# Optimization experiments

Measured on AMD Instinct MI355X. Metric: run time of the kernel, lower is better.

## Reference

```python
import jax, jax.numpy as jnp
import numpy as np

EPS = float(np.finfo(np.float32).eps)
FFT_SIZE, HOP, WIN = 1024, 120, 600
ANCHOR, KF = 7, 7
LRELU_SLOPE = 0.1

def make_log_shift(anchor=ANCHOR, kf=KF, out_scale=1000.0, in_scale=0.001):
    s = (np.arange(kf) + 1) / anchor
    ls = out_scale * np.log(in_scale * s)
    ls -= ls[anchor - 1]
    return -ls  # positive, monotonically decreasing to 0 at the anchor tap

SHIFTS = make_log_shift()

def stft_mag(y):
    # y: (B, T) -> (B, 513, n_frames), matches torch.stft(center=True, reflect)
    B, T = y.shape
    pad = FFT_SIZE // 2
    yp = jnp.pad(y, ((0, 0), (pad, pad)), mode='reflect')
    n_frames = 1 + (T + 2 * pad - FFT_SIZE) // HOP
    idx = jnp.arange(n_frames)[:, None] * HOP + jnp.arange(FFT_SIZE)[None, :]
    frames = yp[:, idx]                                  # (B, n_frames, fft)
    n = np.arange(WIN)
    w = 0.5 * (1.0 - np.cos(2.0 * np.pi * n / WIN))      # periodic Hann(600)
    lp = (FFT_SIZE - WIN) // 2                           # centered pad to fft
    w = jnp.asarray(np.pad(w, (lp, FFT_SIZE - WIN - lp)), dtype=y.dtype)
    spec = jnp.fft.rfft(frames * w, axis=-1)
    mag = jnp.sqrt(jnp.clip(spec.real ** 2 + spec.imag ** 2, EPS))
    return jnp.transpose(mag, (0, 2, 1))

def int_shift(x, k):
    # output[..., f, :] = x[..., f-k, :], zero-fill; k >= 0 (static python int)
    F = x.shape[2]
    if k == 0:
        return x
    if k >= F:
        return jnp.zeros_like(x)
    return jnp.pad(x[:, :, :F - k, :], ((0, 0), (0, 0), (k, 0), (0, 0)))

def frac_shift(x, s):
    # linear-interpolation frequency shift (= interp_shift CUDA kernel)
    if s == int(s):
        return int_shift(x, int(s))
    s0 = int(np.floor(s)); frac = float(s - s0)
    return (1.0 - frac) * int_shift(x, s0) + frac * int_shift(x, s0 + 1)

def wnorm(v, g):
    # weight_norm: w = g * v / ||v|| (norm over all dims but out-channel)
    n = jnp.sqrt(jnp.sum(v * v, axis=(1, 2, 3), keepdims=True))
    return g * v / n

def conv2d(x, w, b, stride, padding):
    out = jax.lax.conv_general_dilated(
        x, w, window_strides=stride,
        padding=((padding[0], padding[0]), (padding[1], padding[1])),
        dimension_numbers=('NCHW', 'OIHW', 'NCHW'))
    return out + b[None, :, None, None]

def lrelu(x):
    return jax.nn.leaky_relu(x, LRELU_SLOPE)

def harmonic_conv(x, v, g, b):
    # x: (B,1,F,T). Log-harmonic lowering: stack 7 fractionally-shifted copies
    lowered = jnp.concatenate([frac_shift(x, SHIFTS[fk]) for fk in range(KF)], axis=1)
    w = wnorm(v, g)                                      # (32, 7, 1, 7)
    return conv2d(lowered, w, b, (1, 1), (0, 3))         # padding[0] forced to 0

def setup_inputs() -> dict:
    key = jax.random.key(0)
    ks = jax.random.split(key, 16)
    p = {}
    p['y'] = jax.random.normal(ks[0], (4, 1, 96000), dtype=jnp.float32)
    p['v0'] = jax.random.normal(ks[1], (32, 7, 1, 7), dtype=jnp.float32) * 0.05
    p['g0'] = jnp.ones((32, 1, 1, 1), dtype=jnp.float32)
    p['b0'] = jnp.zeros((32,), dtype=jnp.float32)
    for i, kk in zip((1, 2, 3), (2, 3, 4)):
        p[f'v{i}'] = jax.random.normal(ks[kk], (32, 32, 3, 9), dtype=jnp.float32) * 0.05
        p[f'g{i}'] = jnp.ones((32, 1, 1, 1), dtype=jnp.float32)
        p[f'b{i}'] = jnp.zeros((32,), dtype=jnp.float32)
    p['v4'] = jax.random.normal(ks[5], (32, 32, 3, 3), dtype=jnp.float32) * 0.05
    p['g4'] = jnp.ones((32, 1, 1, 1), dtype=jnp.float32)
    p['b4'] = jnp.zeros((32,), dtype=jnp.float32)
    p['vo'] = jax.random.normal(ks[6], (1, 32, 3, 3), dtype=jnp.float32) * 0.05
    p['go'] = jnp.ones((1, 1, 1, 1), dtype=jnp.float32)
    p['bo'] = jnp.zeros((1,), dtype=jnp.float32)
    return p

def reference(y, v0, g0, b0, v1, g1, b1, v2, g2, b2, v3, g3, b3,
              v4, g4, b4, vo, go, bo):
    mag = stft_mag(y[:, 0, :])          # (B, 513, frames)
    x = mag[:, None]                    # (B, 1, 513, frames)
    fmap = []
    x = lrelu(harmonic_conv(x, v0, g0, b0)); fmap.append(x)
    x = lrelu(conv2d(x, wnorm(v1, g1), b1, (1, 2), (1, 4))); fmap.append(x)
    x = lrelu(conv2d(x, wnorm(v2, g2), b2, (1, 2), (1, 4))); fmap.append(x)
    x = lrelu(conv2d(x, wnorm(v3, g3), b3, (1, 2), (1, 4))); fmap.append(x)
    x = lrelu(conv2d(x, wnorm(v4, g4), b4, (1, 1), (1, 1))); fmap.append(x)
    x = conv2d(x, wnorm(vo, go), bo, (1, 1), (1, 1)); fmap.append(x)
    flat = x.reshape(x.shape[0], -1)
    return (flat,) + tuple(fmap)
```

## Files before the change

kernel.cpp:

```cpp
#include <hip/hip_runtime.h>
#include <math.h>

#define T_SAMPLES 96000
#define NFRAMES 801
#define NBINS 513
#define FROWS 515
#define EPS32 1.1920928955078125e-07f

typedef _Float16 f16;
typedef f16 f16x2 __attribute__((ext_vector_type(2)));
typedef f16 f16x4 __attribute__((ext_vector_type(4)));
typedef f16 f16x8 __attribute__((ext_vector_type(8)));
typedef float f32x4 __attribute__((ext_vector_type(4)));
typedef float f32x16 __attribute__((ext_vector_type(16)));

__global__ __launch_bounds__(512) void stft_kernel(const float* __restrict__ y,
                                                   float* __restrict__ mag)
{
    int t = blockIdx.x;
    int b = blockIdx.y;
    int tid = threadIdx.x;

    __shared__ float2 buf[2][1024];

    const float* yb = y + (size_t)b * T_SAMPLES;
    for (int n = tid; n < 1024; n += 512) {
        int j = t * 120 + n - 512;
        if (j < 0) j = -j;
        if (j >= T_SAMPLES) j = 2 * T_SAMPLES - 2 - j;
        float v = yb[j];
        int np_ = n - 212;
        float w = 0.0f;
        if (np_ >= 0 && np_ < 600)
            w = 0.5f * (1.0f - cospif((float)np_ * (1.0f / 300.0f)));
        buf[0][n] = make_float2(v * w, 0.0f);
    }
    __syncthreads();

    int srcb = 0;
    #pragma unroll
    for (int stage = 0; stage < 10; ++stage) {
        int m  = 1 << stage;
        int jm = (tid >> stage) << stage;
        float jf = (float)jm * (1.0f / 512.0f);
        float wr = cospif(jf);
        float wi = -sinpif(jf);
        float2 a  = buf[srcb][tid];
        float2 bb = buf[srcb][tid + 512];
        float2 s  = make_float2(a.x + bb.x, a.y + bb.y);
        float2 d  = make_float2(a.x - bb.x, a.y - bb.y);
        float2 dw = make_float2(d.x * wr - d.y * wi, d.x * wi + d.y * wr);
        buf[srcb ^ 1][tid + jm]     = s;
        buf[srcb ^ 1][tid + jm + m] = dw;
        __syncthreads();
        srcb ^= 1;
    }

    float2 v = buf[srcb][tid];
    float msq = v.x * v.x + v.y * v.y;
    mag[((size_t)b * NBINS + tid) * NFRAMES + t] = sqrtf(fmaxf(msq, EPS32));
    if (tid == 0) {
        float2 v5 = buf[srcb][512];
        float m5 = v5.x * v5.x + v5.y * v5.y;
        mag[((size_t)b * NBINS + 512) * NFRAMES + t] = sqrtf(fmaxf(m5, EPS32));
    }
}

__global__ __launch_bounds__(256) void prep_kernel(
    const float* __restrict__ v0, const float* __restrict__ g0,
    const float* __restrict__ v1, const float* __restrict__ g1,
    const float* __restrict__ v2, const float* __restrict__ g2,
    const float* __restrict__ v3, const float* __restrict__ g3,
    const float* __restrict__ v4, const float* __restrict__ g4,
    const float* __restrict__ vo, const float* __restrict__ go,
    float* __restrict__ w0n, float* __restrict__ won,
    f16* __restrict__ A1, f16* __restrict__ A2,
    f16* __restrict__ A3, f16* __restrict__ A4,
    f16* __restrict__ f0c, f16* __restrict__ f1c, f16* __restrict__ f2c,
    f16* __restrict__ f3c, f16* __restrict__ f4c)
{
    int blk = blockIdx.x;
    int tid = threadIdx.x;

    if (blk >= 161) {
        int zb = blk - 161;
        const int TPs[5]   = {840, 456, 264, 136, 136};
        const int tails[5] = {840, 420, 228, 133, 136};
        f16* ptrs[5] = {f0c, f1c, f2c, f3c, f4c};
        f16x8 z;
        #pragma unroll
        for (int j = 0; j < 8; ++j) z[j] = (f16)0.f;
        for (int l = 0; l < 5; ++l) {
            f16* p = ptrs[l];
            int TP = TPs[l], tail = tails[l];
            int rowSlots   = TP * 4;
            int guardSlots = 8 * rowSlots;
            int tailCols   = TP - tail;
            int tailSlots  = 4 * FROWS * tailCols * 4;
            int total = guardSlots + tailSlots;
            for (int i = zb * 256 + tid; i < total; i += 256 * 256) {
                size_t slot;
                if (i < guardSlots) {
                    int rs = i / rowSlots;
                    int q  = i - rs * rowSlots;
                    int b  = rs >> 1;
                    int r  = (rs & 1) ? (FROWS - 1) : 0;
                    slot = ((size_t)(b * FROWS + r)) * rowSlots + q;
                } else {
                    int j2 = i - guardSlots;
                    int per = tailCols * 4;
                    int row = j2 / per;
                    int q   = j2 - row * per;
                    slot = ((size_t)row * TP + tail) * 4 + q;
                }
                *reinterpret_cast<f16x8*>((char*)p + slot * 16) = z;
            }
        }
        return;
    }

    const float *v, *g; f16* Ap = nullptr; float* outf = nullptr;
    int o, per_o, KW = 9;
    if (blk < 32)        { v = v1; g = g1; Ap = A1; o = blk;       per_o = 864; }
    else if (blk < 64)   { v = v2; g = g2; Ap = A2; o = blk - 32;  per_o = 864; }
    else if (blk < 96)   { v = v3; g = g3; Ap = A3; o = blk - 64;  per_o = 864; }
    else if (blk < 128)  { v = v4; g = g4; Ap = A4; o = blk - 96;  per_o = 288; KW = 3; }
    else if (blk < 160)  { v = v0; g = g0; outf = w0n; o = blk - 128; per_o = 49; }
    else                 { v = vo; g = go; outf = won; o = 0;        per_o = 288; }

    const float* vv = v + (size_t)o * per_o;
    __shared__ float red[256];
    float s = 0.f;
    for (int i = tid; i < per_o; i += 256) { float x = vv[i]; s = fmaf(x, x, s); }
    red[tid] = s;
    __syncthreads();
    for (int k = 128; k > 0; k >>= 1) {
        if (tid < k) red[tid] += red[tid + k];
        __syncthreads();
    }
    float scale = g[o] / sqrtf(red[0]);

    if (outf) {
        for (int i = tid; i < per_o; i += 256)
            outf[(size_t)o * per_o + i] = vv[i] * scale;
    } else {
        for (int i = tid; i < per_o; i += 256) {
            int tap = i >> 5;
            int c   = i & 31;
            int df  = tap / KW, kw = tap - df * KW;
            float val = vv[(c * 3 + df) * KW + kw] * scale;
            int l = ((c >> 3) & 1) * 32 + o;
            int ch = c >> 4;
            int j = c & 7;
            Ap[(((tap * 2 + ch) * 64 + l) << 3) + j] = (f16)val;
        }
    }
}

__global__ __launch_bounds__(256) void harmonic_kernel(const float* __restrict__ mag,
                                                       const float* __restrict__ wn,
                                                       const float* __restrict__ bias,
                                                       float* __restrict__ out,
                                                       f16* __restrict__ f0c,
                                                       float fr4, float fr5)
{
    int f = blockIdx.x;
    int b = blockIdx.y;
    int tid = threadIdx.x;

    __shared__ float rows[3][808];

    const float* mb = mag + (size_t)b * NBINS * NFRAMES;

    for (int i = tid; i < 808; i += 256) {
        int tt = i - 3;
        bool ok = (tt >= 0) && (tt < NFRAMES);
        float m336 = (ok && f >= 336) ? mb[(size_t)(f - 336) * NFRAMES + tt] : 0.f;
        float m337 = (ok && f >= 337) ? mb[(size_t)(f - 337) * NFRAMES + tt] : 0.f;
        float m154 = (ok && f >= 154) ? mb[(size_t)(f - 154) * NFRAMES + tt] : 0.f;
        float m155 = (ok && f >= 155) ? mb[(size_t)(f - 155) * NFRAMES + tt] : 0.f;
        float m0   = ok ? mb[(size_t)f * NFRAMES + tt] : 0.f;
        rows[0][i] = (1.f - fr4) * m336 + fr4 * m337;
        rows[1][i] = (1.f - fr5) * m154 + fr5 * m155;
        rows[2][i] = m0;
    }
    __syncthreads();

    char* crow = (char*)f0c + ((size_t)(b * FROWS + f + 1)) * 840 * 64;

    if (tid < 16) {
        int tg = tid >> 2, q = tid & 3;
        int swz = (((tg >> 1) & 3) << 4) | (((tg >> 3) & 1) << 6);
        f16x8 z;
        #pragma unroll
        for (int j = 0; j < 8; ++j) z[j] = (f16)0.f;
        *reinterpret_cast<f16x8*>(crow + ((tg * 64 + q * 16) ^ swz)) = z;
    }

    #pragma unroll
    for (int chunk = 0; chunk < 4; ++chunk) {
        int t = chunk * 256 + tid;
        if (t < NFRAMES) {
            float win[3][7];
            #pragma unroll
            for (int r = 0; r < 3; ++r)
                #pragma unroll
                for (int k = 0; k < 7; ++k)
                    win[r][k] = rows[r][t + k];

            float vals[32];
            #pragma unroll
            for (int o = 0; o < 32; ++o) {
                float a = bias[o];
                #pragma unroll
                for (int r = 0; r < 3; ++r) {
                    const float* wr = wn + (o * 7 + 4 + r) * 7;
                    #pragma unroll
                    for (int kw = 0; kw < 7; ++kw)
                        a = fmaf(win[r][kw], wr[kw], a);
                }
                vals[o] = (a > 0.f) ? a : 0.1f * a;
            }

            #pragma unroll
            for (int o = 0; o < 32; ++o)
                out[(((size_t)b * 32 + o) * NBINS + f) * (size_t)NFRAMES + t] = vals[o];

            int tg = t + 4;
            int swz = (((tg >> 1) & 3) << 4) | (((tg >> 3) & 1) << 6);
            #pragma unroll
            for (int q = 0; q < 4; ++q) {
                f16x8 h;
                #pragma unroll
                for (int j = 0; j < 8; ++j) h[j] = (f16)vals[q * 8 + j];
                *reinterpret_cast<f16x8*>(crow + ((tg * 64 + q * 16) ^ swz)) = h;
            }
        } else if (t < 836) {
            int tg = t + 4;
            int swz = (((tg >> 1) & 3) << 4) | (((tg >> 3) & 1) << 6);
            f16x8 z;
            #pragma unroll
            for (int j = 0; j < 8; ++j) z[j] = (f16)0.f;
            #pragma unroll
            for (int q = 0; q < 4; ++q)
                *reinterpret_cast<f16x8*>(crow + ((tg * 64 + q * 16) ^ swz)) = z;
        }
    }
}

template<int KW, int STRIDE, int PW, int PAD_IN, int PAD_OUT, int NTB, int MINW, bool DO_LRELU>
__global__ __launch_bounds__(256, MINW) void conv_v6(
    const f16* __restrict__ inC, const f16* __restrict__ Ap,
    const float* __restrict__ bias, float* __restrict__ out,
    f16* __restrict__ outC, int Tout, int TpadIn, int TpadOut)
{
    constexpr int NT    = 64;
    constexpr int TR    = NT * STRIDE + KW - 1;
    constexpr int TRP   = (TR + 1) & ~1;
    constexpr int ROWB  = TRP * 64;
    constexpr int SLR   = TRP * 4;
    constexpr int SL    = 6 * SLR;
    constexpr int KPT   = (SL + 255) / 256;
    constexpr int TOFF  = (PAD_IN - PW) & 15;
    constexpr int NFOFF = 32 * STRIDE * 64;

    __shared__ char ldsb[KPT * 256 * 16];

    const int tid  = threadIdx.x;
    const int lane = tid & 63;
    const int wave = tid >> 6;

    const int NWG = NTB * 129 * 4;
    int lin = blockIdx.x;
    int xcd = lin & 7, sl = lin >> 3;
    const int q = NWG / 8, r = NWG % 8;
    int work = (xcd < r ? xcd * (q + 1) : r * (q + 1) + (xcd - r) * q) + sl;
    const int tb   = work % NTB;
    int rem        = work / NTB;
    const int fblk = rem % 129;
    const int b    = rem / 129;
    const int f0   = fblk * 4;
    const int brow = b * FROWS + f0;
    const int t0   = tb * NT;
    const int base_t = t0 * STRIDE + (PAD_IN - PW);

    {
        const char* inB = (const char*)inC;
        #pragma unroll
        for (int k = 0; k < KPT; ++k) {
            int s  = tid + k * 256;
            int fr = s / SLR;
            int s2 = s - fr * SLR;
            __builtin_amdgcn_global_load_lds(
                (const __attribute__((address_space(1))) void*)
                    (inB + ((size_t)(brow + fr) * TpadIn + base_t) * 64 + (size_t)s2 * 16),
                (__attribute__((address_space(3))) void*)
                    (ldsb + (k * 256 + (tid & 192)) * 16),
                16, 0, 0);
        }
    }

    const int tln = lane & 31;
    const int hi  = lane >> 5;
    int baddr0[KW];
    #pragma unroll
    for (int kw = 0; kw < KW; ++kw) {
        int trow = tln * STRIDE + kw;
        int x = trow + TOFF;
        int swz = (((x >> 1) & 3) << 4) | (((x >> 3) & 1) << 6);
        baddr0[kw] = (trow * 64 + hi * 16) ^ swz;
    }

    float bs[16];
    #pragma unroll
    for (int rr = 0; rr < 16; ++rr) bs[rr] = bias[4 * hi + 8 * (rr >> 2) + (rr & 3)];

    __syncthreads();

    f32x16 acc[2];
    #pragma unroll
    for (int nf = 0; nf < 2; ++nf)
        #pragma unroll
        for (int rr = 0; rr < 16; ++rr) acc[nf][rr] = 0.f;

    const char* lrow = ldsb + wave * ROWB;
    #pragma unroll
    for (int df = 0; df < 3; ++df) {
        f16x8 a[KW * 2];
        #pragma unroll
        for (int kw = 0; kw < KW; ++kw)
            #pragma unroll
            for (int ch = 0; ch < 2; ++ch)
                a[kw * 2 + ch] = *reinterpret_cast<const f16x8*>(
                    Ap + (((df * KW + kw) * 2 + ch) << 9) + lane * 8);
        #pragma unroll
        for (int kw = 0; kw < KW; ++kw)
            #pragma unroll
            for (int ch = 0; ch < 2; ++ch)
                #pragma unroll
                for (int nf = 0; nf < 2; ++nf) {
                    f16x8 bf = *reinterpret_cast<const f16x8*>(
                        lrow + ((baddr0[kw] ^ (ch << 5)) + df * ROWB + nf * NFOFF));
                    acc[nf] = __builtin_amdgcn_mfma_f32_32x32x16_f16(a[kw * 2 + ch], bf, acc[nf], 0, 0, 0);
                }
    }

    const int f = f0 + wave;
    if (f >= NBINS) return;

    char* crow = nullptr;
    if constexpr (PAD_OUT > 0)
        crow = (char*)outC + ((size_t)(b * FROWS + f + 1)) * TpadOut * 64;

    #pragma unroll
    for (int nf = 0; nf < 2; ++nf) {
        int t = t0 + nf * 32 + tln;
        bool vt = (t < Tout);
        float vals[16];
        #pragma unroll
        for (int rr = 0; rr < 16; ++rr) {
            float v = acc[nf][rr] + bs[rr];
            if (DO_LRELU) v = (v > 0.f) ? v : 0.1f * v;
            vals[rr] = v;
        }
        if (vt) {
            #pragma unroll
            for (int rr = 0; rr < 16; ++rr) {
                int o = 4 * hi + 8 * (rr >> 2) + (rr & 3);
                out[(((size_t)b * 32 + o) * NBINS + f) * Tout + t] = vals[rr];
            }
        }
        if constexpr (PAD_OUT > 0) {
            int tg = t + PAD_OUT;
            int swz = (((tg >> 1) & 3) << 4) | (((tg >> 3) & 1) << 6);
            int rowbyte = (tg * 64) ^ swz;
            #pragma unroll
            for (int qq = 0; qq < 4; ++qq) {
                f16x4 hv;
                #pragma unroll
                for (int rr = 0; rr < 4; ++rr)
                    hv[rr] = vt ? (f16)vals[4 * qq + rr] : (f16)0.f;
                *reinterpret_cast<f16x4*>(crow + (rowbyte ^ ((4 * hi + 8 * qq) << 1))) = hv;
            }
        }
    }
    if constexpr (PAD_OUT > 0) {
        if (tb == 0 && lane < PAD_OUT * 4) {
            int tgp = lane >> 2, oct = lane & 3;
            f16x8 z;
            #pragma unroll
            for (int j = 0; j < 8; ++j) z[j] = (f16)0.f;
            *reinterpret_cast<f16x8*>(crow + tgp * 64 + oct * 16) = z;
        }
    }
}

__global__ __launch_bounds__(256) void convo_v2(const f16* __restrict__ inC,
                                                const float* __restrict__ won,
                                                const float* __restrict__ bias,
                                                float* __restrict__ f5,
                                                float* __restrict__ flat)
{
    const int TP4 = 136;
    int blk = blockIdx.x;
    int b = blk / 257, fp = blk - (b * 257);
    int tid = threadIdx.x;
    int f = fp * 2 + (tid >> 7);
    int t = tid & 127;
    if (f >= NBINS || t >= 101) return;

    float acc = bias[0];
    #pragma unroll
    for (int df = 0; df < 3; ++df) {
        const char* row = (const char*)inC + ((size_t)(b * FROWS + f + df)) * TP4 * 64;
        #pragma unroll
        for (int kw = 0; kw < 3; ++kw) {
            int tg = t + kw;
            int swz = (((tg >> 1) & 3) << 4) | (((tg >> 3) & 1) << 6);
            #pragma unroll
            for (int q2 = 0; q2 < 4; ++q2) {
                f16x8 h = *reinterpret_cast<const f16x8*>(row + ((tg * 64 + q2 * 16) ^ swz));
                #pragma unroll
                for (int j = 0; j < 8; ++j)
                    acc = fmaf((float)h[j], won[((q2 * 8 + j) * 3 + df) * 3 + kw], acc);
            }
        }
    }
    size_t idx = ((size_t)(b * NBINS + f)) * 101 + t;
    f5[idx] = acc;
    flat[idx] = acc;
}

extern "C" void kernel_launch(void* const* d_in, const int* in_sizes, int n_in,
                              void* d_out, int out_size, void* d_ws, size_t ws_size,
                              hipStream_t stream)
{
    const float* y  = (const float*)d_in[0];
    const float* v0 = (const float*)d_in[1];
    const float* g0 = (const float*)d_in[2];
    const float* b0 = (const float*)d_in[3];
    const float* v1 = (const float*)d_in[4];
    const float* g1 = (const float*)d_in[5];
    const float* b1 = (const float*)d_in[6];
    const float* v2 = (const float*)d_in[7];
    const float* g2 = (const float*)d_in[8];
    const float* b2 = (const float*)d_in[9];
    const float* v3 = (const float*)d_in[10];
    const float* g3 = (const float*)d_in[11];
    const float* b3 = (const float*)d_in[12];
    const float* v4 = (const float*)d_in[13];
    const float* g4 = (const float*)d_in[14];
    const float* b4 = (const float*)d_in[15];
    const float* vo = (const float*)d_in[16];
    const float* go = (const float*)d_in[17];
    const float* bo = (const float*)d_in[18];

    float* out = (float*)d_out;
    float* ws  = (float*)d_ws;

    const size_t SFLAT = (size_t)4 * NBINS * 101;
    const size_t NF0   = (size_t)4 * 32 * NBINS * 801;
    const size_t NF1   = (size_t)4 * 32 * NBINS * 401;
    const size_t NF2   = (size_t)4 * 32 * NBINS * 201;
    const size_t NF3   = (size_t)4 * 32 * NBINS * 101;
    float* oflat = out;
    float* f0 = out + SFLAT;
    float* f1 = f0 + NF0;
    float* f2 = f1 + NF1;
    float* f3 = f2 + NF2;
    float* f4 = f3 + NF3;
    float* f5 = f4 + NF3;

    float* mag = f1;

    const int TP0 = 840, TP1 = 456, TP2 = 264, TP3 = 136, TP4 = 136;
    size_t off = 0;
    float* w0n = ws + off; off += 1568;
    float* won = ws + off; off += 288;
    f16* A1 = (f16*)(ws + off);
    f16* A2 = A1 + 27648;
    f16* A3 = A2 + 27648;
    f16* A4 = A3 + 27648;
    f16* f0c = A4 + 9216;
    f16* f1c = f0c + (size_t)4 * FROWS * TP0 * 32;
    f16* f2c = f1c + (size_t)4 * FROWS * TP1 * 32;
    f16* f3c = f2c + (size_t)4 * FROWS * TP2 * 32;
    f16* f4c = f3c + (size_t)4 * FROWS * TP3 * 32;

    prep_kernel<<<417, 256, 0, stream>>>(v0, g0, v1, g1, v2, g2, v3, g3,
                                         v4, g4, vo, go, w0n, won,
                                         A1, A2, A3, A4,
                                         f0c, f1c, f2c, f3c, f4c);

    stft_kernel<<<dim3(NFRAMES, 4), 512, 0, stream>>>(y, mag);

    double sh4 = -(1000.0 * log(0.001 * (5.0 / 7.0)) - 1000.0 * log(0.001));
    double sh5 = -(1000.0 * log(0.001 * (6.0 / 7.0)) - 1000.0 * log(0.001));
    float fr4 = (float)(sh4 - floor(sh4));
    float fr5 = (float)(sh5 - floor(sh5));

    harmonic_kernel<<<dim3(NBINS, 4), 256, 0, stream>>>(mag, w0n, b0, f0, f0c, fr4, fr5);

    conv_v6<9, 2, 4, 4, 4, 7, 3, true><<<7 * 129 * 4, 256, 0, stream>>>(f0c, A1, b1, f1, f1c, 401, TP0, TP1);
    conv_v6<9, 2, 4, 4, 4, 4, 3, true><<<4 * 129 * 4, 256, 0, stream>>>(f1c, A2, b2, f2, f2c, 201, TP1, TP2);
    conv_v6<9, 2, 4, 4, 5, 2, 3, true><<<2 * 129 * 4, 256, 0, stream>>>(f2c, A3, b3, f3, f3c, 101, TP2, TP3);
    conv_v6<3, 1, 1, 5, 1, 2, 4, true><<<2 * 129 * 4, 256, 0, stream>>>(f3c, A4, b4, f4, f4c, 101, TP3, TP4);

    convo_v2<<<257 * 4, 256, 0, stream>>>(f4c, won, bo, f5, oflat);
}
```

Measured before the change: 401.4 us.

## Pack two real frames per complex FFT and batch frames per block

The STFT kernel is rewritten so each wavefront transforms two real frames at once, packed as the real and imaginary parts of one complex 1024-point FFT. The two spectra are then separated with the conjugate-symmetry identity, and each block handles 8 frames. Magnitudes are staged in shared memory and written with vectorised 16-byte stores into a frame dimension padded to 804, which the harmonic kernel now reads with the new stride. The goal is to halve FFT work, reduce block count and sync overhead, and make the frame-major stores coalesced. The risk is that the padded layout needs a larger mag buffer, and the buffer allocation is not visible here.

```diff
diff --git a/kernel.cpp b/kernel.cpp
--- a/kernel.cpp
+++ b/kernel.cpp
@@ -5,6 +5,7 @@
 #define NFRAMES 801
 #define NBINS 513
 #define FROWS 515
+#define MAGT 804
 #define EPS32 1.1920928955078125e-07f
 
 typedef _Float16 f16;
@@ -14,55 +15,87 @@
 typedef float f32x4 __attribute__((ext_vector_type(4)));
 typedef float f32x16 __attribute__((ext_vector_type(16)));
 
-__global__ __launch_bounds__(512) void stft_kernel(const float* __restrict__ y,
-                                                   float* __restrict__ mag)
+__global__ __launch_bounds__(256) void stft_v2(const float* __restrict__ y,
+                                               float* __restrict__ mag)
 {
-    int t = blockIdx.x;
-    int b = blockIdx.y;
-    int tid = threadIdx.x;
-
-    __shared__ float2 buf[2][1024];
-
+    __shared__ float2 fft[2][4][1024];
+    float* mg = (float*)&fft[1][0][0];
+    const int MGS = 520;
+
+    const int tid  = threadIdx.x;
+    const int lane = tid & 63;
+    const int wv   = tid >> 6;
+    const int t0   = blockIdx.x * 8;
+    const int b    = blockIdx.y;
     const float* yb = y + (size_t)b * T_SAMPLES;
-    for (int n = tid; n < 1024; n += 512) {
-        int j = t * 120 + n - 512;
-        if (j < 0) j = -j;
-        if (j >= T_SAMPLES) j = 2 * T_SAMPLES - 2 - j;
-        float v = yb[j];
+
+    const int tA = t0 + 2 * wv;
+    for (int n = lane; n < 1024; n += 64) {
+        float w = 0.f;
         int np_ = n - 212;
-        float w = 0.0f;
         if (np_ >= 0 && np_ < 600)
             w = 0.5f * (1.0f - cospif((float)np_ * (1.0f / 300.0f)));
-        buf[0][n] = make_float2(v * w, 0.0f);
+        int j1 = tA * 120 + n - 512;
+        if (j1 < 0) j1 = -j1;
+        if (j1 >= T_SAMPLES) j1 = 2 * T_SAMPLES - 2 - j1;
+        int j2 = j1 + 120;
+        {
+            int jj = tA * 120 + 120 + n - 512;
+            if (jj < 0) jj = -jj;
+            if (jj >= T_SAMPLES) jj = 2 * T_SAMPLES - 2 - jj;
+            j2 = jj;
+        }
+        fft[0][wv][n] = make_float2(w * yb[j1], w * yb[j2]);
     }
     __syncthreads();
 
     int srcb = 0;
     #pragma unroll
     for (int stage = 0; stage < 10; ++stage) {
-        int m  = 1 << stage;
-        int jm = (tid >> stage) << stage;
-        float jf = (float)jm * (1.0f / 512.0f);
-        float wr = cospif(jf);
-        float wi = -sinpif(jf);
-        float2 a  = buf[srcb][tid];
-        float2 bb = buf[srcb][tid + 512];
-        float2 s  = make_float2(a.x + bb.x, a.y + bb.y);
-        float2 d  = make_float2(a.x - bb.x, a.y - bb.y);
-        float2 dw = make_float2(d.x * wr - d.y * wi, d.x * wi + d.y * wr);
-        buf[srcb ^ 1][tid + jm]     = s;
-        buf[srcb ^ 1][tid + jm + m] = dw;
+        int m = 1 << stage;
+        #pragma unroll
+        for (int it = 0; it < 8; ++it) {
+            int idx = lane + it * 64;
+            int jm  = (idx >> stage) << stage;
+            float jf = (float)jm * (1.0f / 512.0f);
+            float wr = cospif(jf);
+            float wi = -sinpif(jf);
+            float2 a  = fft[srcb][wv][idx];
+            float2 bb = fft[srcb][wv][idx + 512];
+            float2 s  = make_float2(a.x + bb.x, a.y + bb.y);
+            float2 d  = make_float2(a.x - bb.x, a.y - bb.y);
+            float2 dw = make_float2(d.x * wr - d.y * wi, d.x * wi + d.y * wr);
+            fft[srcb ^ 1][wv][idx + jm]     = s;
+            fft[srcb ^ 1][wv][idx + jm + m] = dw;
+        }
         __syncthreads();
         srcb ^= 1;
     }
 
-    float2 v = buf[srcb][tid];
-    float msq = v.x * v.x + v.y * v.y;
-    mag[((size_t)b * NBINS + tid) * NFRAMES + t] = sqrtf(fmaxf(msq, EPS32));
-    if (tid == 0) {
-        float2 v5 = buf[srcb][512];
-        float m5 = v5.x * v5.x + v5.y * v5.y;
-        mag[((size_t)b * NBINS + 512) * NFRAMES + t] = sqrtf(fmaxf(m5, EPS32));
+    for (int k = lane; k < 513; k += 64) {
+        float2 zk = fft[0][wv][k];
+        float2 zr = fft[0][wv][(1024 - k) & 1023];
+        float x1r = 0.5f * (zk.x + zr.x);
+        float x1i = 0.5f * (zk.y - zr.y);
+        float x2r = 0.5f * (zk.y + zr.y);
+        float x2i = 0.5f * (zr.x - zk.x);
+        mg[(2 * wv)     * MGS + k] = sqrtf(fmaxf(x1r * x1r + x1i * x1i, EPS32));
+        mg[(2 * wv + 1) * MGS + k] = sqrtf(fmaxf(x2r * x2r + x2i * x2i, EPS32));
+    }
+    __syncthreads();
+
+    for (int f = tid; f < 513; f += 256) {
+        size_t base = ((size_t)(b * NBINS) + f) * MAGT + t0;
+        if (t0 + 7 < NFRAMES) {
+            f32x4 v0 = {mg[0 * MGS + f], mg[1 * MGS + f], mg[2 * MGS + f], mg[3 * MGS + f]};
+            f32x4 v1 = {mg[4 * MGS + f], mg[5 * MGS + f], mg[6 * MGS + f], mg[7 * MGS + f]};
+            *reinterpret_cast<f32x4*>(&mag[base])     = v0;
+            *reinterpret_cast<f32x4*>(&mag[base + 4]) = v1;
+        } else {
+            #pragma unroll
+            for (int p = 0; p < 8; ++p)
+                if (t0 + p < NFRAMES) mag[base + p] = mg[p * MGS + f];
+        }
     }
 }
 
@@ -170,16 +203,16 @@
 
     __shared__ float rows[3][808];
 
-    const float* mb = mag + (size_t)b * NBINS * NFRAMES;
+    const float* mb = mag + (size_t)b * NBINS * MAGT;
 
     for (int i = tid; i < 808; i += 256) {
         int tt = i - 3;
         bool ok = (tt >= 0) && (tt < NFRAMES);
-        float m336 = (ok && f >= 336) ? mb[(size_t)(f - 336) * NFRAMES + tt] : 0.f;
-        float m337 = (ok && f >= 337) ? mb[(size_t)(f - 337) * NFRAMES + tt] : 0.f;
-        float m154 = (ok && f >= 154) ? mb[(size_t)(f - 154) * NFRAMES + tt] : 0.f;
-        float m155 = (ok && f >= 155) ? mb[(size_t)(f - 155) * NFRAMES + tt] : 0.f;
-        float m0   = ok ? mb[(size_t)f * NFRAMES + tt] : 0.f;
+        float m336 = (ok && f >= 336) ? mb[(size_t)(f - 336) * MAGT + tt] : 0.f;
+        float m337 = (ok && f >= 337) ? mb[(size_t)(f - 337) * MAGT + tt] : 0.f;
+        float m154 = (ok && f >= 154) ? mb[(size_t)(f - 154) * MAGT + tt] : 0.f;
+        float m155 = (ok && f >= 155) ? mb[(size_t)(f - 155) * MAGT + tt] : 0.f;
+        float m0   = ok ? mb[(size_t)f * MAGT + tt] : 0.f;
         rows[0][i] = (1.f - fr4) * m336 + fr4 * m337;
         rows[1][i] = (1.f - fr5) * m154 + fr5 * m155;
         rows[2][i] = m0;
@@ -492,7 +525,7 @@
                                          A1, A2, A3, A4,
                                          f0c, f1c, f2c, f3c, f4c);
 
-    stft_kernel<<<dim3(NFRAMES, 4), 512, 0, stream>>>(y, mag);
+    stft_v2<<<dim3(101, 4), 256, 0, stream>>>(y, mag);
 
     double sh4 = -(1000.0 * log(0.001 * (5.0 / 7.0)) - 1000.0 * log(0.001));
     double sh5 = -(1000.0 * log(0.001 * (6.0 / 7.0)) - 1000.0 * log(0.001));
```

Measured after the change: 392.6 us. -2.2%, faster.
